# Performance work log

Measured on AMD Instinct MI355X. Metric: run time of the kernel, lower is better.

## Reference

```python
import jax, jax.numpy as jnp
import numpy as np

N = 100000       # nodes
E = 1600000      # edges
V = 50000        # vocab
H = 256          # embedding dim (hsize)
A = 64           # per-head out dim (asize)
NH = 3           # num_heads
G = 64           # graphs in batch


def setup_inputs() -> dict:
    key = jax.random.key(0)
    ks = jax.random.split(key, 12)
    h0 = jax.random.randint(ks[0], (N,), 0, V)
    src = jax.random.randint(ks[1], (E,), 0, N)
    dst = jax.random.randint(ks[2], (E,), 0, N)
    graph_ids = jnp.sort(jax.random.randint(ks[3], (N,), 0, G))
    s = 0.05
    emb = jax.random.normal(ks[4], (V, H), jnp.float32) * s
    W_fc = jax.random.normal(ks[5], (H, NH * A), jnp.float32) * s   # GATConv fc
    attn_l = jax.random.normal(ks[6], (NH, A), jnp.float32) * s
    attn_r = jax.random.normal(ks[7], (NH, A), jnp.float32) * s
    bias_gat = jax.random.normal(ks[8], (NH, A), jnp.float32) * s
    W1 = jax.random.normal(ks[9], (A, 128), jnp.float32) * s
    b1 = jnp.zeros((128,), jnp.float32)
    W2 = jax.random.normal(ks[10], (128, 16), jnp.float32) * s
    b2 = jnp.zeros((16,), jnp.float32)
    return dict(h0=h0, src=src, dst=dst, graph_ids=graph_ids, emb=emb,
                W_fc=W_fc, attn_l=attn_l, attn_r=attn_r, bias_gat=bias_gat,
                W1=W1, b1=b1, W2=W2, b2=b2)


def reference(h0, src, dst, graph_ids, emb, W_fc, attn_l, attn_r, bias_gat,
              W1, b1, W2, b2):
    # embedding lookup
    h1 = emb[h0]                                            # [N, H]
    # GATConv: linear projection per head
    feat = (h1 @ W_fc).reshape(N, NH, A)                    # [N, NH, A]
    el = jnp.einsum('nha,ha->nh', feat, attn_l)             # [N, NH]
    er = jnp.einsum('nha,ha->nh', feat, attn_r)             # [N, NH]
    e = jax.nn.leaky_relu(el[src] + er[dst], 0.2)           # [E, NH]
    # segment softmax over incoming edges of each dst node
    m = jax.ops.segment_max(e, dst, num_segments=N)         # [N, NH]
    e_exp = jnp.exp(e - m[dst])                             # [E, NH]
    denom = jax.ops.segment_sum(e_exp, dst, num_segments=N) # [N, NH]
    alpha = e_exp / denom[dst]                              # [E, NH]
    # scatter-aggregate messages
    msg = alpha[:, :, None] * feat[src]                     # [E, NH, A]
    rst = jax.ops.segment_sum(msg, dst, num_segments=N)     # [N, NH, A]
    rst = rst + bias_gat[None]                              # GATConv bias
    # relu + mean over heads
    h2 = jnp.mean(jax.nn.relu(rst), axis=1)                 # [N, A]
    # MLP predictor: ReLU then Identity
    h3 = jax.nn.relu(h2 @ W1 + b1) @ W2 + b2                # [N, 16]
    # dgl.mean_nodes: per-graph mean readout
    sums = jax.ops.segment_sum(h3, graph_ids, num_segments=G)            # [G, 16]
    counts = jax.ops.segment_sum(jnp.ones((N,), h3.dtype), graph_ids, num_segments=G)
    return sums / jnp.maximum(counts, 1.0)[:, None]         # [G, 16]
```

## Files before the change

### kernel.cpp

```cpp
#include <hip/hip_runtime.h>
#include <hip/hip_bf16.h>

#define NNODES 100000
#define NEDGES 1600000
#define VOCAB 50000
#define HDIM 256
#define ADIM 64
#define NHEADS 3
#define FDIM 192
#define NGRAPH 64
#define NPART 64

typedef __attribute__((ext_vector_type(8))) short bf16x8;
typedef __attribute__((ext_vector_type(4))) float f32x4;

__device__ __forceinline__ float bf2f(unsigned short u) {
  return __uint_as_float((unsigned int)u << 16);
}
__device__ __forceinline__ unsigned short f2bf(float f) {
  unsigned int u = __float_as_uint(f);
  u += 0x7FFFu + ((u >> 16) & 1u);
  return (unsigned short)(u >> 16);
}

__global__ __launch_bounds__(256) void conv_weights_kernel(
    const float* __restrict__ Wfc, const float* __restrict__ W1,
    const float* __restrict__ W2, unsigned short* __restrict__ Wt,
    unsigned short* __restrict__ W1t, unsigned short* __restrict__ W2t)
{
  int i = blockIdx.x * 256 + threadIdx.x;
  if (i < HDIM * FDIM) {
    int c = i / HDIM, k = i % HDIM;
    Wt[i] = f2bf(Wfc[(size_t)k * FDIM + c]);
  } else if (i < HDIM * FDIM + 128 * 64) {
    int j = i - HDIM * FDIM;
    int c = j / 64, k = j % 64;
    W1t[j] = f2bf(W1[(size_t)k * 128 + c]);
  } else if (i < HDIM * FDIM + 128 * 64 + 16 * 128) {
    int j = i - HDIM * FDIM - 128 * 64;
    int c = j / 128, k = j % 128;
    W2t[j] = f2bf(W2[(size_t)k * 16 + c]);
  }
}

__global__ __launch_bounds__(256) void proj_gemm_kernel(
    const float* __restrict__ emb,
    const unsigned short* __restrict__ Wt,
    const float* __restrict__ attn_l,
    const float* __restrict__ attn_r,
    unsigned short* __restrict__ proj_bf,
    float4* __restrict__ elv4, float4* __restrict__ erv4, int V)
{
  const int wave = threadIdx.x >> 6;
  const int lane = threadIdx.x & 63;
  const int row0 = blockIdx.x * 64 + wave * 16;
  const int cb = lane & 15;
  const int q  = lane >> 4;
  int arow = row0 + cb;
  if (arow >= V) arow = V - 1;
  const int kgrp = q * 8;

  f32x4 acc[12];
#pragma unroll
  for (int c = 0; c < 12; ++c) acc[c] = (f32x4){0.f, 0.f, 0.f, 0.f};

  const float* arow_p = &emb[(size_t)arow * HDIM + kgrp];
  const unsigned short* bcol_p = &Wt[(size_t)cb * HDIM + kgrp];

#pragma unroll
  for (int ks = 0; ks < 8; ++ks) {
    float4 f0 = *reinterpret_cast<const float4*>(arow_p + ks * 32);
    float4 f1 = *reinterpret_cast<const float4*>(arow_p + ks * 32 + 4);
    bf16x8 a;
    a[0] = (short)f2bf(f0.x); a[1] = (short)f2bf(f0.y);
    a[2] = (short)f2bf(f0.z); a[3] = (short)f2bf(f0.w);
    a[4] = (short)f2bf(f1.x); a[5] = (short)f2bf(f1.y);
    a[6] = (short)f2bf(f1.z); a[7] = (short)f2bf(f1.w);
#pragma unroll
    for (int c = 0; c < 12; ++c) {
      bf16x8 b = *reinterpret_cast<const bf16x8*>(bcol_p + (size_t)c * 16 * HDIM + ks * 32);
      acc[c] = __builtin_amdgcn_mfma_f32_16x16x32_bf16(a, b, acc[c], 0, 0, 0);
    }
  }

  const int rb = row0 + 4 * q;
#pragma unroll
  for (int i = 0; i < 4; ++i) {
    int r = rb + i;
    if (r < V) {
#pragma unroll
      for (int c = 0; c < 12; ++c)
        proj_bf[(size_t)r * FDIM + c * 16 + cb] = f2bf(acc[c][i]);
    }
  }

  float al_v[12], ar_v[12];
#pragma unroll
  for (int c = 0; c < 12; ++c) {
    al_v[c] = attn_l[c * 16 + cb];
    ar_v[c] = attn_r[c * 16 + cb];
  }
  float elp[4][3], erp[4][3];
#pragma unroll
  for (int i = 0; i < 4; ++i)
#pragma unroll
    for (int h = 0; h < 3; ++h) {
      float sl = 0.f, sr = 0.f;
#pragma unroll
      for (int cc = 0; cc < 4; ++cc) {
        float v = acc[h * 4 + cc][i];
        sl += v * al_v[h * 4 + cc];
        sr += v * ar_v[h * 4 + cc];
      }
      elp[i][h] = sl; erp[i][h] = sr;
    }
#pragma unroll
  for (int s = 8; s > 0; s >>= 1) {
#pragma unroll
    for (int i = 0; i < 4; ++i)
#pragma unroll
      for (int h = 0; h < 3; ++h) {
        elp[i][h] += __shfl_xor(elp[i][h], s, 64);
        erp[i][h] += __shfl_xor(erp[i][h], s, 64);
      }
  }
  if (cb == 0) {
#pragma unroll
    for (int i = 0; i < 4; ++i) {
      int r = rb + i;
      if (r < V) {
        elv4[r] = make_float4(elp[i][0], elp[i][1], elp[i][2], 0.f);
        erv4[r] = make_float4(erp[i][0], erp[i][1], erp[i][2], 0.f);
      }
    }
  }
}

__global__ __launch_bounds__(256) void hist_kernel(
    const int* __restrict__ dst, int* __restrict__ cnt,
    unsigned short* __restrict__ rank16, int E)
{
  int e = blockIdx.x * 256 + threadIdx.x;
  if (e < E) rank16[e] = (unsigned short)atomicAdd(&cnt[dst[e]], 1);
}

__global__ __launch_bounds__(256) void scan_sum_kernel(
    const int* __restrict__ cnt, int* __restrict__ bsum, int n)
{
  __shared__ int red[256];
  int t = threadIdx.x;
  int base = blockIdx.x * 1024 + t * 4;
  int s = 0;
#pragma unroll
  for (int j = 0; j < 4; ++j) if (base + j < n) s += cnt[base + j];
  red[t] = s;
  __syncthreads();
  for (int o = 128; o > 0; o >>= 1) {
    if (t < o) red[t] += red[t + o];
    __syncthreads();
  }
  if (t == 0) bsum[blockIdx.x] = red[0];
}

__global__ void scan_bsum_kernel(int* bsum, int nb)
{
  if (threadIdx.x == 0 && blockIdx.x == 0) {
    int acc = 0;
    for (int i = 0; i < nb; ++i) { int v = bsum[i]; bsum[i] = acc; acc += v; }
  }
}

__global__ __launch_bounds__(256) void scan_write_kernel(
    const int* __restrict__ cnt, const int* __restrict__ bsum,
    int* __restrict__ offs, int n, int total)
{
  __shared__ int sd[256];
  int t = threadIdx.x;
  int base = blockIdx.x * 1024 + t * 4;
  int c[4];
  int ts = 0;
#pragma unroll
  for (int j = 0; j < 4; ++j) { c[j] = (base + j < n) ? cnt[base + j] : 0; ts += c[j]; }
  sd[t] = ts;
  __syncthreads();
  for (int o = 1; o < 256; o <<= 1) {
    int v = (t >= o) ? sd[t - o] : 0;
    __syncthreads();
    sd[t] += v;
    __syncthreads();
  }
  int run = sd[t] - ts + bsum[blockIdx.x];
#pragma unroll
  for (int j = 0; j < 4; ++j) {
    if (base + j < n) offs[base + j] = run;
    run += c[j];
  }
  if (blockIdx.x == 0 && t == 0) offs[n] = total;
}

__global__ __launch_bounds__(256) void scatter_kernel(
    const int* __restrict__ src, const int* __restrict__ dst,
    const int* __restrict__ h0, const unsigned short* __restrict__ rank16,
    const int* __restrict__ offs, unsigned short* __restrict__ recs16, int E)
{
  int e = blockIdx.x * 256 + threadIdx.x;
  if (e >= E) return;
  int p = offs[dst[e]] + (int)rank16[e];
  recs16[p] = (unsigned short)h0[src[e]];
}

__global__ __launch_bounds__(256) void aggregate_kernel(
    const unsigned short* __restrict__ recs16, const int* __restrict__ offs,
    const int* __restrict__ h0,
    const unsigned short* __restrict__ proj_bf,
    const float4* __restrict__ elv4, const float4* __restrict__ erv4,
    const float* __restrict__ bias_gat,
    unsigned short* __restrict__ h2bf, int N)
{
  int lane = threadIdx.x & 63;
  int n = blockIdx.x * 4 + (threadIdx.x >> 6);
  if (n >= N) return;
  const float4 ero = erv4[h0[n]];
  int lo = offs[n], hi = offs[n + 1];
  float a0 = 0.f, a1 = 0.f, a2 = 0.f, d0 = 0.f, d1 = 0.f, d2 = 0.f;

  int i = lo;
  for (; i + 4 <= hi; i += 4) {
    int vs[4];
#pragma unroll
    for (int j = 0; j < 4; ++j) vs[j] = recs16[i + j];
    float4 ev[4];
#pragma unroll
    for (int j = 0; j < 4; ++j) ev[j] = elv4[vs[j]];
    const unsigned short* ps[4];
#pragma unroll
    for (int j = 0; j < 4; ++j) ps[j] = &proj_bf[(size_t)vs[j] * FDIM];
    float g0[4], g1[4], g2[4];
#pragma unroll
    for (int j = 0; j < 4; ++j) {
      g0[j] = bf2f(ps[j][lane]);
      g1[j] = bf2f(ps[j][64 + lane]);
      g2[j] = bf2f(ps[j][128 + lane]);
    }
#pragma unroll
    for (int j = 0; j < 4; ++j) {
      float e0 = ev[j].x + ero.x, e1 = ev[j].y + ero.y, e2 = ev[j].z + ero.z;
      e0 = e0 > 0.f ? e0 : 0.2f * e0;
      e1 = e1 > 0.f ? e1 : 0.2f * e1;
      e2 = e2 > 0.f ? e2 : 0.2f * e2;
      float w0 = __expf(e0), w1 = __expf(e1), w2 = __expf(e2);
      a0 += w0 * g0[j]; a1 += w1 * g1[j]; a2 += w2 * g2[j];
      d0 += w0; d1 += w1; d2 += w2;
    }
  }
  for (; i < hi; ++i) {
    int vs = recs16[i];
    float4 ev = elv4[vs];
    const unsigned short* ps = &proj_bf[(size_t)vs * FDIM];
    float e0 = ev.x + ero.x, e1 = ev.y + ero.y, e2 = ev.z + ero.z;
    e0 = e0 > 0.f ? e0 : 0.2f * e0;
    e1 = e1 > 0.f ? e1 : 0.2f * e1;
    e2 = e2 > 0.f ? e2 : 0.2f * e2;
    float w0 = __expf(e0), w1 = __expf(e1), w2 = __expf(e2);
    a0 += w0 * bf2f(ps[lane]);
    a1 += w1 * bf2f(ps[64 + lane]);
    a2 += w2 * bf2f(ps[128 + lane]);
    d0 += w0; d1 += w1; d2 += w2;
  }

  float i0 = d0 > 0.f ? 1.f / d0 : 0.f;
  float i1 = d1 > 0.f ? 1.f / d1 : 0.f;
  float i2 = d2 > 0.f ? 1.f / d2 : 0.f;
  float r0 = a0 * i0 + bias_gat[lane];
  float r1 = a1 * i1 + bias_gat[64 + lane];
  float r2 = a2 * i2 + bias_gat[128 + lane];
  float h2 = (fmaxf(r0, 0.f) + fmaxf(r1, 0.f) + fmaxf(r2, 0.f)) * (1.f / 3.f);
  h2bf[(size_t)n * 64 + lane] = f2bf(h2);
}

__global__ __launch_bounds__(256) void post_mfma_kernel(
    const unsigned short* __restrict__ h2bf,
    const unsigned short* __restrict__ W1t,
    const float* __restrict__ b1,
    const unsigned short* __restrict__ W2t,
    const float* __restrict__ b2, const int* __restrict__ gid,
    float* __restrict__ sums_priv, float* __restrict__ counts_priv, int N)
{
  __shared__ unsigned short z_lds[64 * 128];
  const int wave = threadIdx.x >> 6;
  const int lane = threadIdx.x & 63;
  const int r = lane & 15;
  const int q = lane >> 4;
  const int kg = q * 8;
  const int rw0 = blockIdx.x * 64 + wave * 16;

  int arow = rw0 + r;
  if (arow >= N) arow = N - 1;

  f32x4 acc1[8];
#pragma unroll
  for (int c = 0; c < 8; ++c) acc1[c] = (f32x4){0.f, 0.f, 0.f, 0.f};

#pragma unroll
  for (int ks = 0; ks < 2; ++ks) {
    bf16x8 a = *reinterpret_cast<const bf16x8*>(&h2bf[(size_t)arow * 64 + kg + ks * 32]);
#pragma unroll
    for (int c = 0; c < 8; ++c) {
      bf16x8 b = *reinterpret_cast<const bf16x8*>(&W1t[(size_t)(c * 16 + r) * 64 + kg + ks * 32]);
      acc1[c] = __builtin_amdgcn_mfma_f32_16x16x32_bf16(a, b, acc1[c], 0, 0, 0);
    }
  }
#pragma unroll
  for (int c = 0; c < 8; ++c) {
    float bb = b1[c * 16 + r];
#pragma unroll
    for (int i = 0; i < 4; ++i) {
      float z = acc1[c][i] + bb;
      z = z > 0.f ? z : 0.f;
      z_lds[(wave * 16 + 4 * q + i) * 128 + c * 16 + r] = f2bf(z);
    }
  }
  __syncthreads();

  f32x4 acc2 = (f32x4){0.f, 0.f, 0.f, 0.f};
#pragma unroll
  for (int ks = 0; ks < 4; ++ks) {
    bf16x8 a = *reinterpret_cast<const bf16x8*>(&z_lds[(wave * 16 + r) * 128 + kg + ks * 32]);
    bf16x8 b = *reinterpret_cast<const bf16x8*>(&W2t[(size_t)r * 128 + kg + ks * 32]);
    acc2 = __builtin_amdgcn_mfma_f32_16x16x32_bf16(a, b, acc2, 0, 0, 0);
  }
  const int part = blockIdx.x & (NPART - 1);
  float bb2 = b2[r];
#pragma unroll
  for (int i = 0; i < 4; ++i) {
    int row = rw0 + 4 * q + i;
    if (row < N) {
      int g = gid[row];
      atomicAdd(&sums_priv[(part * NGRAPH + g) * 16 + r], acc2[i] + bb2);
      if (r == 0) atomicAdd(&counts_priv[part * NGRAPH + g], 1.f);
    }
  }
}

__global__ void finalize_kernel(const float* __restrict__ sums_priv,
                                const float* __restrict__ counts_priv,
                                float* __restrict__ out)
{
  int j = threadIdx.x;
  int g = j >> 4;
  float s = 0.f, c = 0.f;
  for (int p = 0; p < NPART; ++p) {
    s += sums_priv[p * NGRAPH * 16 + j];
    c += counts_priv[p * NGRAPH + g];
  }
  out[j] = s / fmaxf(c, 1.f);
}

extern "C" void kernel_launch(void* const* d_in, const int* in_sizes, int n_in,
                              void* d_out, int out_size, void* d_ws, size_t ws_size,
                              hipStream_t stream)
{
  const int*   h0  = (const int*)  d_in[0];
  const int*   src = (const int*)  d_in[1];
  const int*   dst = (const int*)  d_in[2];
  const int*   gid = (const int*)  d_in[3];
  const float* emb = (const float*)d_in[4];
  const float* Wfc = (const float*)d_in[5];
  const float* al  = (const float*)d_in[6];
  const float* ar  = (const float*)d_in[7];
  const float* bg  = (const float*)d_in[8];
  const float* W1  = (const float*)d_in[9];
  const float* b1  = (const float*)d_in[10];
  const float* W2  = (const float*)d_in[11];
  const float* b2  = (const float*)d_in[12];
  float* out = (float*)d_out;

  char* ws = (char*)d_ws;
  size_t off = 0;
  auto alloc = [&](size_t bytes) -> void* {
    off = (off + 255) & ~(size_t)255;
    void* p = ws + off;
    off += bytes;
    return p;
  };
  unsigned short* Wt      = (unsigned short*)alloc((size_t)FDIM * HDIM * 2);
  unsigned short* W1t     = (unsigned short*)alloc((size_t)128 * 64 * 2);
  unsigned short* W2t     = (unsigned short*)alloc((size_t)16 * 128 * 2);
  unsigned short* proj_bf = (unsigned short*)alloc((size_t)VOCAB * FDIM * 2);
  unsigned short* h2bf    = (unsigned short*)alloc((size_t)NNODES * 64 * 2);
  unsigned short* recs16  = (unsigned short*)alloc((size_t)NEDGES * 2);
  unsigned short* rank16  = (unsigned short*)alloc((size_t)NEDGES * 2);
  float4* elv4   = (float4*)alloc((size_t)VOCAB * 16);
  float4* erv4   = (float4*)alloc((size_t)VOCAB * 16);
  int*    cnt    = (int*)   alloc((size_t)NNODES * 4);
  int*    offs   = (int*)   alloc((size_t)(NNODES + 1) * 4);
  int*    bsum   = (int*)   alloc((size_t)128 * 4);
  float*  sums   = (float*) alloc((size_t)NPART * NGRAPH * 16 * 4);
  float*  cnts   = (float*) alloc((size_t)NPART * NGRAPH * 4);

  hipMemsetAsync(cnt,  0, (size_t)NNODES * 4, stream);
  hipMemsetAsync(sums, 0, (size_t)NPART * NGRAPH * 16 * 4, stream);
  hipMemsetAsync(cnts, 0, (size_t)NPART * NGRAPH * 4, stream);

  const int NB = (NNODES + 1023) / 1024;

  conv_weights_kernel<<<(HDIM * FDIM + 128 * 64 + 16 * 128 + 255) / 256, 256, 0, stream>>>(
      Wfc, W1, W2, Wt, W1t, W2t);
  proj_gemm_kernel<<<(VOCAB + 63) / 64, 256, 0, stream>>>(emb, Wt, al, ar,
                                                          proj_bf, elv4, erv4, VOCAB);
  hist_kernel<<<(NEDGES + 255) / 256, 256, 0, stream>>>(dst, cnt, rank16, NEDGES);
  scan_sum_kernel<<<NB, 256, 0, stream>>>(cnt, bsum, NNODES);
  scan_bsum_kernel<<<1, 64, 0, stream>>>(bsum, NB);
  scan_write_kernel<<<NB, 256, 0, stream>>>(cnt, bsum, offs, NNODES, NEDGES);
  scatter_kernel<<<(NEDGES + 255) / 256, 256, 0, stream>>>(src, dst, h0, rank16, offs,
                                                           recs16, NEDGES);
  aggregate_kernel<<<(NNODES + 3) / 4, 256, 0, stream>>>(recs16, offs, h0, proj_bf,
                                                         elv4, erv4, bg, h2bf, NNODES);
  post_mfma_kernel<<<(NNODES + 63) / 64, 256, 0, stream>>>(h2bf, W1t, b1, W2t, b2, gid,
                                                           sums, cnts, NNODES);
  finalize_kernel<<<1, 1024, 0, stream>>>(sums, cnts, out);
}
```

Before: 356.9 us.

## Precompute per-edge softmax weights in a thread-per-node kernel before aggregation

Splits the aggregation into two kernels. A new thread-per-node kernel computes the leaky-relu and exp of the attention logits once per edge, packs the source id with three bf16 weights into an 8-byte record, and stores the per-node reciprocal denominators. Before this, all 64 lanes of the aggregate wave redundantly computed the same exps per edge. The trade-off is an extra launch, a 12.8MB write and reread of the packed records, and bf16 rounding of the weights, with load imbalance possible in the thread-per-node pass.

```diff
diff --git a/kernel.cpp b/kernel.cpp
--- a/kernel.cpp
+++ b/kernel.cpp
@@ -209,32 +209,57 @@
   recs16[p] = (unsigned short)h0[src[e]];
 }
 
-__global__ __launch_bounds__(256) void aggregate_kernel(
+__global__ __launch_bounds__(256) void wexp_kernel(
     const unsigned short* __restrict__ recs16, const int* __restrict__ offs,
     const int* __restrict__ h0,
-    const unsigned short* __restrict__ proj_bf,
     const float4* __restrict__ elv4, const float4* __restrict__ erv4,
-    const float* __restrict__ bias_gat,
+    uint2* __restrict__ wrec, float4* __restrict__ inv4, int N)
+{
+  int n = blockIdx.x * 256 + threadIdx.x;
+  if (n >= N) return;
+  const float4 ero = erv4[h0[n]];
+  int lo = offs[n], hi = offs[n + 1];
+  float d0 = 0.f, d1 = 0.f, d2 = 0.f;
+  for (int p = lo; p < hi; ++p) {
+    unsigned v = recs16[p];
+    float4 ev = elv4[v];
+    float e0 = ev.x + ero.x, e1 = ev.y + ero.y, e2 = ev.z + ero.z;
+    e0 = e0 > 0.f ? e0 : 0.2f * e0;
+    e1 = e1 > 0.f ? e1 : 0.2f * e1;
+    e2 = e2 > 0.f ? e2 : 0.2f * e2;
+    unsigned short u0 = f2bf(__expf(e0));
+    unsigned short u1 = f2bf(__expf(e1));
+    unsigned short u2 = f2bf(__expf(e2));
+    d0 += bf2f(u0); d1 += bf2f(u1); d2 += bf2f(u2);
+    wrec[p] = make_uint2(v | ((unsigned)u0 << 16),
+                         (unsigned)u1 | ((unsigned)u2 << 16));
+  }
+  inv4[n] = make_float4(d0 > 0.f ? 1.f / d0 : 0.f,
+                        d1 > 0.f ? 1.f / d1 : 0.f,
+                        d2 > 0.f ? 1.f / d2 : 0.f, 0.f);
+}
+
+__global__ __launch_bounds__(256) void aggregate_kernel(
+    const uint2* __restrict__ wrec, const int* __restrict__ offs,
+    const float4* __restrict__ inv4,
+    const unsigned short* __restrict__ proj_bf, const float* __restrict__ bias_gat,
     unsigned short* __restrict__ h2bf, int N)
 {
   int lane = threadIdx.x & 63;
   int n = blockIdx.x * 4 + (threadIdx.x >> 6);
   if (n >= N) return;
-  const float4 ero = erv4[h0[n]];
   int lo = offs[n], hi = offs[n + 1];
-  float a0 = 0.f, a1 = 0.f, a2 = 0.f, d0 = 0.f, d1 = 0.f, d2 = 0.f;
+  float a0 = 0.f, a1 = 0.f, a2 = 0.f;
 
   int i = lo;
   for (; i + 4 <= hi; i += 4) {
-    int vs[4];
-#pragma unroll
-    for (int j = 0; j < 4; ++j) vs[j] = recs16[i + j];
-    float4 ev[4];
-#pragma unroll
-    for (int j = 0; j < 4; ++j) ev[j] = elv4[vs[j]];
+    uint2 r[4];
+#pragma unroll
+    for (int j = 0; j < 4; ++j) r[j] = wrec[i + j];
     const unsigned short* ps[4];
 #pragma unroll
-    for (int j = 0; j < 4; ++j) ps[j] = &proj_bf[(size_t)vs[j] * FDIM];
+    for (int j = 0; j < 4; ++j)
+      ps[j] = &proj_bf[(size_t)(r[j].x & 0xFFFFu) * FDIM];
     float g0[4], g1[4], g2[4];
 #pragma unroll
     for (int j = 0; j < 4; ++j) {
@@ -244,36 +269,23 @@
     }
 #pragma unroll
     for (int j = 0; j < 4; ++j) {
-      float e0 = ev[j].x + ero.x, e1 = ev[j].y + ero.y, e2 = ev[j].z + ero.z;
-      e0 = e0 > 0.f ? e0 : 0.2f * e0;
-      e1 = e1 > 0.f ? e1 : 0.2f * e1;
-      e2 = e2 > 0.f ? e2 : 0.2f * e2;
-      float w0 = __expf(e0), w1 = __expf(e1), w2 = __expf(e2);
-      a0 += w0 * g0[j]; a1 += w1 * g1[j]; a2 += w2 * g2[j];
-      d0 += w0; d1 += w1; d2 += w2;
+      a0 += bf2f((unsigned short)(r[j].x >> 16)) * g0[j];
+      a1 += bf2f((unsigned short)(r[j].y & 0xFFFFu)) * g1[j];
+      a2 += bf2f((unsigned short)(r[j].y >> 16)) * g2[j];
     }
   }
   for (; i < hi; ++i) {
-    int vs = recs16[i];
-    float4 ev = elv4[vs];
-    const unsigned short* ps = &proj_bf[(size_t)vs * FDIM];
-    float e0 = ev.x + ero.x, e1 = ev.y + ero.y, e2 = ev.z + ero.z;
-    e0 = e0 > 0.f ? e0 : 0.2f * e0;
-    e1 = e1 > 0.f ? e1 : 0.2f * e1;
-    e2 = e2 > 0.f ? e2 : 0.2f * e2;
-    float w0 = __expf(e0), w1 = __expf(e1), w2 = __expf(e2);
-    a0 += w0 * bf2f(ps[lane]);
-    a1 += w1 * bf2f(ps[64 + lane]);
-    a2 += w2 * bf2f(ps[128 + lane]);
-    d0 += w0; d1 += w1; d2 += w2;
-  }
-
-  float i0 = d0 > 0.f ? 1.f / d0 : 0.f;
-  float i1 = d1 > 0.f ? 1.f / d1 : 0.f;
-  float i2 = d2 > 0.f ? 1.f / d2 : 0.f;
-  float r0 = a0 * i0 + bias_gat[lane];
-  float r1 = a1 * i1 + bias_gat[64 + lane];
-  float r2 = a2 * i2 + bias_gat[128 + lane];
+    uint2 r = wrec[i];
+    const unsigned short* ps = &proj_bf[(size_t)(r.x & 0xFFFFu) * FDIM];
+    a0 += bf2f((unsigned short)(r.x >> 16)) * bf2f(ps[lane]);
+    a1 += bf2f((unsigned short)(r.y & 0xFFFFu)) * bf2f(ps[64 + lane]);
+    a2 += bf2f((unsigned short)(r.y >> 16)) * bf2f(ps[128 + lane]);
+  }
+
+  const float4 inv = inv4[n];
+  float r0 = a0 * inv.x + bias_gat[lane];
+  float r1 = a1 * inv.y + bias_gat[64 + lane];
+  float r2 = a2 * inv.z + bias_gat[128 + lane];
   float h2 = (fmaxf(r0, 0.f) + fmaxf(r1, 0.f) + fmaxf(r2, 0.f)) * (1.f / 3.f);
   h2bf[(size_t)n * 64 + lane] = f2bf(h2);
 }
@@ -390,8 +402,10 @@
   unsigned short* h2bf    = (unsigned short*)alloc((size_t)NNODES * 64 * 2);
   unsigned short* recs16  = (unsigned short*)alloc((size_t)NEDGES * 2);
   unsigned short* rank16  = (unsigned short*)alloc((size_t)NEDGES * 2);
+  uint2*  wrec   = (uint2*) alloc((size_t)NEDGES * 8);
   float4* elv4   = (float4*)alloc((size_t)VOCAB * 16);
   float4* erv4   = (float4*)alloc((size_t)VOCAB * 16);
+  float4* inv4   = (float4*)alloc((size_t)NNODES * 16);
   int*    cnt    = (int*)   alloc((size_t)NNODES * 4);
   int*    offs   = (int*)   alloc((size_t)(NNODES + 1) * 4);
   int*    bsum   = (int*)   alloc((size_t)128 * 4);
@@ -414,8 +428,10 @@
   scan_write_kernel<<<NB, 256, 0, stream>>>(cnt, bsum, offs, NNODES, NEDGES);
   scatter_kernel<<<(NEDGES + 255) / 256, 256, 0, stream>>>(src, dst, h0, rank16, offs,
                                                            recs16, NEDGES);
-  aggregate_kernel<<<(NNODES + 3) / 4, 256, 0, stream>>>(recs16, offs, h0, proj_bf,
-                                                         elv4, erv4, bg, h2bf, NNODES);
+  wexp_kernel<<<(NNODES + 255) / 256, 256, 0, stream>>>(recs16, offs, h0, elv4, erv4,
+                                                        wrec, inv4, NNODES);
+  aggregate_kernel<<<(NNODES + 3) / 4, 256, 0, stream>>>(wrec, offs, inv4, proj_bf,
+                                                         bg, h2bf, NNODES);
   post_mfma_kernel<<<(NNODES + 63) / 64, 256, 0, stream>>>(h2bf, W1t, b1, W2t, b2, gid,
                                                            sums, cnts, NNODES);
   finalize_kernel<<<1, 1024, 0, stream>>>(sums, cnts, out);
```

After: 346.9 us. 1.03x faster.
